# Kernel optimization log

Measured on AMD Instinct MI355X. Metric: run time of the kernel, lower is better.

## Reference

```python
import jax, jax.numpy as jnp
import numpy as np


def setup_inputs() -> dict:
    key = jax.random.key(0)
    k1, k2 = jax.random.split(key)
    batch, d_model, L = 4096, 1024, 2048
    # binary inputs in {0,1} as in torch.randint(0, 2, ...)
    x = jax.random.randint(k1, (batch, L), 0, 2, dtype=jnp.int32)
    references = jax.random.randint(k2, (d_model, L), 0, 2).astype(jnp.float32)
    return {"x": x, "references": references}


def reference(x, references):
    # Hamming distance between binary vectors a,b in {0,1}:
    #   sum(a != b) = sum(a) + sum(b) - 2 * a.b
    # This avoids materializing the (batch, d_model, L) broadcast tensor
    # while computing exactly the same values as the original module.
    L = x.shape[-1]
    xf = x.astype(jnp.float32)                     # (B, L)
    dot = jnp.einsum('bl,dl->bd', xf, references)  # (B, D)
    sum_x = jnp.sum(xf, axis=-1, keepdims=True)    # (B, 1)
    sum_r = jnp.sum(references, axis=-1)           # (D,)
    hamming = sum_x + sum_r[None, :] - 2.0 * dot   # (B, D)
    mean = L / 2
    std = 0.5 * (L ** 0.5)
    return (hamming - mean) / std
```

## Files before the change

kernel.cpp:

```cpp
#include <hip/hip_runtime.h>
#include <stdint.h>

constexpr int B_ROWS = 4096;
constexpr int D_ROWS = 1024;
constexpr int L_LEN  = 2048;

using int32x4 = __attribute__((ext_vector_type(4))) int;

__global__ __launch_bounds__(256) void convert_kernel(
    const int* __restrict__ x, const float* __restrict__ r,
    uint32_t* __restrict__ xq, uint32_t* __restrict__ rq,
    int groups_x, int groups_total)
{
  const int tid = blockIdx.x * blockDim.x + threadIdx.x;
  const int nth = gridDim.x * blockDim.x;
  for (int g = tid; g < groups_total; g += nth) {
    if (g < groups_x) {
      const int4 v = *reinterpret_cast<const int4*>(x + (size_t)g * 4);
      const uint32_t b0 = v.x ? 0xFFu : 0x01u;
      const uint32_t b1 = v.y ? 0xFFu : 0x01u;
      const uint32_t b2 = v.z ? 0xFFu : 0x01u;
      const uint32_t b3 = v.w ? 0xFFu : 0x01u;
      xq[g] = b0 | (b1 << 8) | (b2 << 16) | (b3 << 24);
    } else {
      const int gr = g - groups_x;
      const float4 v = *reinterpret_cast<const float4*>(r + (size_t)gr * 4);
      const uint32_t b0 = (v.x != 0.0f) ? 0xFFu : 0x01u;
      const uint32_t b1 = (v.y != 0.0f) ? 0xFFu : 0x01u;
      const uint32_t b2 = (v.z != 0.0f) ? 0xFFu : 0x01u;
      const uint32_t b3 = (v.w != 0.0f) ? 0xFFu : 0x01u;
      rq[gr] = b0 | (b1 << 8) | (b2 << 16) | (b3 << 24);
    }
  }
}

constexpr int BM = 128;
constexpr int BN = 64;
constexpr int BK = 128;
constexpr int KSTEPS = L_LEN / BK;

typedef __attribute__((address_space(3))) void       as3_void;
typedef const __attribute__((address_space(1))) void as1_cvoid;

__device__ __forceinline__ void gload_lds16(const void* g, void* l) {
  __builtin_amdgcn_global_load_lds((as1_cvoid*)g, (as3_void*)l, 16, 0, 0);
}

__global__ __launch_bounds__(256) void gemm_i8_kernel(
    const char* __restrict__ Aq, const char* __restrict__ Bq,
    float* __restrict__ out)
{
  __shared__ __align__(16) char A_lds[BM * BK];
  __shared__ __align__(16) char B_lds[BN * BK];

  const int t    = threadIdx.x;
  const int lane = t & 63;
  const int w    = t >> 6;
  const int wr   = w >> 1;
  const int wc   = w & 1;
  const int bm   = blockIdx.x * BM;
  const int bn   = blockIdx.y * BN;

  const int l8  = lane >> 3;
  const int c16 = lane & 7;

  int32x4 acc[4][2] = {};

  for (int ks = 0; ks < KSTEPS; ++ks) {
    const int k0 = ks * BK;

#pragma unroll
    for (int c = 0; c < 4; ++c) {
      const int rb = c * 32 + w * 8;
      const int r  = rb + l8;
      const char* g = Aq + (size_t)(bm + r) * L_LEN + k0 + ((c16 ^ (r & 7)) * 16);
      gload_lds16(g, A_lds + rb * BK);
    }
#pragma unroll
    for (int c = 0; c < 2; ++c) {
      const int rb = c * 32 + w * 8;
      const int r  = rb + l8;
      const char* g = Bq + (size_t)(bn + r) * L_LEN + k0 + ((c16 ^ (r & 7)) * 16);
      gload_lds16(g, B_lds + rb * BK);
    }
    __syncthreads();

    int32x4 a[4][2], b[2][2];
#pragma unroll
    for (int kk = 0; kk < 2; ++kk) {
      const int kcol = kk * 64 + (lane >> 4) * 16;
#pragma unroll
      for (int f = 0; f < 4; ++f) {
        const int row = wr * 64 + f * 16 + (lane & 15);
        a[f][kk] = *reinterpret_cast<const int32x4*>(
            A_lds + row * BK + (kcol ^ ((row & 7) << 4)));
      }
#pragma unroll
      for (int gg = 0; gg < 2; ++gg) {
        const int row = wc * 32 + gg * 16 + (lane & 15);
        b[gg][kk] = *reinterpret_cast<const int32x4*>(
            B_lds + row * BK + (kcol ^ ((row & 7) << 4)));
      }
    }
#pragma unroll
    for (int f = 0; f < 4; ++f)
#pragma unroll
      for (int gg = 0; gg < 2; ++gg)
#pragma unroll
        for (int kk = 0; kk < 2; ++kk)
          acc[f][gg] = __builtin_amdgcn_mfma_i32_16x16x64_i8(
              a[f][kk], b[gg][kk], acc[f][gg], 0, 0, 0);
    __syncthreads();
  }

  const float scale = -0.5f * 0.04419417382415922f;
#pragma unroll
  for (int f = 0; f < 4; ++f) {
    const int brow = bm + wr * 64 + f * 16 + (lane >> 4) * 4;
#pragma unroll
    for (int gg = 0; gg < 2; ++gg) {
      const int d = bn + wc * 32 + gg * 16 + (lane & 15);
#pragma unroll
      for (int reg = 0; reg < 4; ++reg)
        out[(size_t)(brow + reg) * D_ROWS + d] = (float)acc[f][gg][reg] * scale;
    }
  }
}

extern "C" void kernel_launch(void* const* d_in, const int* in_sizes, int n_in,
                              void* d_out, int out_size, void* d_ws, size_t ws_size,
                              hipStream_t stream) {
  const int*   x = (const int*)d_in[0];
  const float* r = (const float*)d_in[1];
  float*     out = (float*)d_out;

  char* Aq = (char*)d_ws;
  char* Bq = Aq + (size_t)B_ROWS * L_LEN;

  const int groups_x = B_ROWS * L_LEN / 4;
  const int groups_r = D_ROWS * L_LEN / 4;
  const int groups_total = groups_x + groups_r;

  convert_kernel<<<2048, 256, 0, stream>>>(
      x, r, (uint32_t*)Aq, (uint32_t*)Bq, groups_x, groups_total);

  dim3 grid(B_ROWS / BM, D_ROWS / BN);
  gemm_i8_kernel<<<grid, 256, 0, stream>>>(Aq, Bq, out);
}
```

Baseline: 30.00 us.

## Double-buffer LDS tiles to prefetch next K-step during MFMA compute

Splits the A and B shared-memory tiles into two buffers. The int8 GEMM now issues the asynchronous global-to-LDS loads for the next K-step before computing on the current one, so memory latency can overlap with MFMA work. It also drops one barrier per iteration and hoists the per-thread global address computation out of the loop. The cost is twice the LDS per block, which may lower occupancy, and the end-of-iteration barrier still waits for the prefetch to land.

```diff
diff --git a/kernel.cpp b/kernel.cpp
--- a/kernel.cpp
+++ b/kernel.cpp
@@ -50,8 +50,8 @@
     const char* __restrict__ Aq, const char* __restrict__ Bq,
     float* __restrict__ out)
 {
-  __shared__ __align__(16) char A_lds[BM * BK];
-  __shared__ __align__(16) char B_lds[BN * BK];
+  __shared__ __align__(16) char A_lds[2][BM * BK];
+  __shared__ __align__(16) char B_lds[2][BN * BK];
 
   const int t    = threadIdx.x;
   const int lane = t & 63;
@@ -64,26 +64,34 @@
   const int l8  = lane >> 3;
   const int c16 = lane & 7;
 
+  const char* gA[4];
+#pragma unroll
+  for (int c = 0; c < 4; ++c) {
+    const int r = c * 32 + w * 8 + l8;
+    gA[c] = Aq + (size_t)(bm + r) * L_LEN + ((c16 ^ (r & 7)) * 16);
+  }
+  const char* gB[2];
+#pragma unroll
+  for (int c = 0; c < 2; ++c) {
+    const int r = c * 32 + w * 8 + l8;
+    gB[c] = Bq + (size_t)(bn + r) * L_LEN + ((c16 ^ (r & 7)) * 16);
+  }
+
+#define STAGE(buf, k0) do {                                                   \
+    _Pragma("unroll") for (int _c = 0; _c < 4; ++_c)                          \
+      gload_lds16(gA[_c] + (k0), A_lds[buf] + (_c * 32 + w * 8) * BK);        \
+    _Pragma("unroll") for (int _c = 0; _c < 2; ++_c)                          \
+      gload_lds16(gB[_c] + (k0), B_lds[buf] + (_c * 32 + w * 8) * BK);        \
+  } while (0)
+
   int32x4 acc[4][2] = {};
 
+  STAGE(0, 0);
+  __syncthreads();
+
   for (int ks = 0; ks < KSTEPS; ++ks) {
-    const int k0 = ks * BK;
-
-#pragma unroll
-    for (int c = 0; c < 4; ++c) {
-      const int rb = c * 32 + w * 8;
-      const int r  = rb + l8;
-      const char* g = Aq + (size_t)(bm + r) * L_LEN + k0 + ((c16 ^ (r & 7)) * 16);
-      gload_lds16(g, A_lds + rb * BK);
-    }
-#pragma unroll
-    for (int c = 0; c < 2; ++c) {
-      const int rb = c * 32 + w * 8;
-      const int r  = rb + l8;
-      const char* g = Bq + (size_t)(bn + r) * L_LEN + k0 + ((c16 ^ (r & 7)) * 16);
-      gload_lds16(g, B_lds + rb * BK);
-    }
-    __syncthreads();
+    const int cur = ks & 1;
+    if (ks + 1 < KSTEPS) STAGE(cur ^ 1, (ks + 1) * BK);
 
     int32x4 a[4][2], b[2][2];
 #pragma unroll
@@ -93,13 +101,13 @@
       for (int f = 0; f < 4; ++f) {
         const int row = wr * 64 + f * 16 + (lane & 15);
         a[f][kk] = *reinterpret_cast<const int32x4*>(
-            A_lds + row * BK + (kcol ^ ((row & 7) << 4)));
+            A_lds[cur] + row * BK + (kcol ^ ((row & 7) << 4)));
       }
 #pragma unroll
       for (int gg = 0; gg < 2; ++gg) {
         const int row = wc * 32 + gg * 16 + (lane & 15);
         b[gg][kk] = *reinterpret_cast<const int32x4*>(
-            B_lds + row * BK + (kcol ^ ((row & 7) << 4)));
+            B_lds[cur] + row * BK + (kcol ^ ((row & 7) << 4)));
       }
     }
 #pragma unroll
@@ -110,8 +118,10 @@
         for (int kk = 0; kk < 2; ++kk)
           acc[f][gg] = __builtin_amdgcn_mfma_i32_16x16x64_i8(
               a[f][kk], b[gg][kk], acc[f][gg], 0, 0, 0);
+
     __syncthreads();
   }
+#undef STAGE
 
   const float scale = -0.5f * 0.04419417382415922f;
 #pragma unroll
```

Result: no change. 30.46 us (+1.5%).
